# Performance work log

Measured on AMD Instinct MI355X. Metric: run time of the kernel, lower is better.

## Reference

```python
import jax, jax.numpy as jnp
import numpy as np
from jax import lax

EPS = 1e-5
NUM_HEADS = 8


def _safe_norm(x):
    # sqrt(max(sum x^2, EPS^2)) == max(||x||, EPS); grad-safe at 0
    return jnp.sqrt(jnp.maximum(jnp.sum(x * x, axis=-1, keepdims=True), EPS * EPS))


def _project(x):
    norm = _safe_norm(x)
    max_norm = 1.0 - EPS
    scale = jnp.where(norm >= max_norm, max_norm / (norm + EPS), jnp.ones_like(norm))
    return x * scale


def _logmap0(y):
    # logarithmic_map(0, y): lambda_0 = 2/(1+EPS)
    y = _project(y)
    n = _safe_norm(y)  # clamp(min=EPS) is built in
    lam = 2.0 / (1.0 + EPS)
    return (2.0 / lam) * jnp.arctanh(n) * (y / n)


def _expmap0(v):
    # exponential_map(0, v): lambda_0 = 2/(1+EPS)
    n = _safe_norm(v)
    lam = 2.0 / (1.0 + EPS)
    return _project(jnp.tanh(lam * n / 2.0) * (v / n))


def _mobius_add(x, y):
    x = _project(x)
    y = _project(y)
    xy = jnp.sum(x * y, axis=-1, keepdims=True)
    xn = jnp.sum(x * x, axis=-1, keepdims=True)
    yn = jnp.sum(y * y, axis=-1, keepdims=True)
    num = (1.0 + 2.0 * xy + yn) * x + (1.0 - xn) * y
    den = 1.0 + 2.0 * xy + xn * yn + EPS
    return _project(num / den)


def _hyp_linear(x, W, b):
    # HyperbolicLinear.forward: project -> logmap0 -> linear -> expmap0 -> mobius-add bias
    x = _project(x)
    xt = _logmap0(x)
    t = xt @ W.T
    r = _expmap0(t)
    r = _mobius_add(r, jnp.broadcast_to(b, r.shape))
    return r


def setup_inputs() -> dict:
    key = jax.random.key(0)
    ks = jax.random.split(key, 11)
    B, S, E = 4, 512, 512

    def xavier(k, shape):
        bound = np.sqrt(6.0 / (shape[0] + shape[1]))
        return jax.random.uniform(k, shape, jnp.float32, -bound, bound)

    return {
        "query": jax.random.normal(ks[0], (B, S, E), jnp.float32),
        "key": jax.random.normal(ks[1], (B, S, E), jnp.float32),
        "value": jax.random.normal(ks[2], (B, S, E), jnp.float32),
        "Wq": xavier(ks[3], (E, E)), "bq": 0.01 * jax.random.normal(ks[4], (E,), jnp.float32),
        "Wk": xavier(ks[5], (E, E)), "bk": 0.01 * jax.random.normal(ks[6], (E,), jnp.float32),
        "Wv": xavier(ks[7], (E, E)), "bv": 0.01 * jax.random.normal(ks[8], (E,), jnp.float32),
        "Wo": xavier(ks[9], (E, E)), "bo": 0.01 * jax.random.normal(ks[10], (E,), jnp.float32),
    }


def reference(query, key, value, Wq, bq, Wk, bk, Wv, bv, Wo, bo):
    B, S, E = query.shape
    H = NUM_HEADS
    D = E // H

    Q = _hyp_linear(query, Wq, bq).reshape(B, S, H, D).transpose(0, 2, 1, 3)  # [B,H,S,D]
    K = _hyp_linear(key, Wk, bk).reshape(B, S, H, D).transpose(0, 2, 1, 3)
    V = _hyp_linear(value, Wv, bv).reshape(B, S, H, D).transpose(0, 2, 1, 3)

    # Pairwise Poincare distance: d(q,k) = acosh(1 + 2||q-k||^2/((1-|q|^2)(1-|k|^2)) + EPS)
    q = _project(Q)
    k = _project(K)
    qn = jnp.sum(q * q, axis=-1)  # [B,H,S]
    kn = jnp.sum(k * k, axis=-1)  # [B,H,S]
    qk = jnp.einsum('bhqd,bhkd->bhqk', q, k)
    num = jnp.maximum(qn[..., :, None] + kn[..., None, :] - 2.0 * qk, 0.0)
    den = jnp.maximum((1.0 - qn)[..., :, None] * (1.0 - kn)[..., None, :], EPS)
    dist = jnp.arccosh(1.0 + 2.0 * num / den + EPS)  # [B,H,Sq,Sk]
    attn = jax.nn.softmax(-dist, axis=-1)

    # Sequential Mobius-add accumulation over key/value positions
    wt = jnp.moveaxis(attn, 3, 0)  # [Sk,B,H,Sq]
    vt = jnp.moveaxis(V, 2, 0)     # [Sk,B,H,D]

    @jax.checkpoint
    def step(ws, wv):
        wj, vj = wv  # wj: [B,H,Sq], vj: [B,H,D]
        return _mobius_add(ws, wj[..., None] * vj[:, :, None, :]), None

    ws0 = jnp.zeros((B, H, S, D), query.dtype)
    attended, _ = lax.scan(step, ws0, (wt, vt))  # [B,H,Sq,D]

    attended = attended.transpose(0, 2, 1, 3).reshape(B, S, E)
    return _hyp_linear(attended, Wo, bo)
```

## Files before the change

kernel.cpp:

```cpp
#include <hip/hip_runtime.h>
#include <math.h>

#define EPS  1e-5f
#define EPS2 1e-10f
#define MAXN (1.0f - EPS)

using short8  = __attribute__((ext_vector_type(8))) short;
using floatx4 = __attribute__((ext_vector_type(4))) float;
using float2v = __attribute__((ext_vector_type(2))) float;

template <int CTRL>
static __device__ __forceinline__ float qperm(float x) {
  return __int_as_float(__builtin_amdgcn_update_dpp(
      __float_as_int(x), __float_as_int(x), CTRL, 0xF, 0xF, false));
}
#define QP_XOR1    0xB1
#define QP_XOR2    0x4E
#define QP_HALFMIR 0x141

#if __has_builtin(__builtin_elementwise_fma)
static __device__ __forceinline__ float2v fma2(float2v a, float2v b, float2v c) {
  return __builtin_elementwise_fma(a, b, c);
}
#else
static __device__ __forceinline__ float2v fma2(float2v a, float2v b, float2v c) {
  float2v r; r.x = fmaf(a.x, b.x, c.x); r.y = fmaf(a.y, b.y, c.y); return r;
}
#endif

static __device__ __forceinline__ int pack_hi2(float a, float b) {
  return (int)((__float_as_uint(a) >> 16) | (__float_as_uint(b) & 0xFFFF0000u));
}
static __device__ __forceinline__ float hi_of(float a) {
  return __uint_as_float(__float_as_uint(a) & 0xFFFF0000u);
}

static __device__ __forceinline__ float logmap_f(float ss) {
  const float r = sqrtf(fmaxf(ss, EPS2));
  float at;
  if (r >= MAXN) {
    at = 0.5f * logf((r * (2.0f - EPS) + EPS) / (EPS * (1.0f + r)));
  } else {
    at = 0.5f * logf((1.0f + r) / (1.0f - r));
  }
  return (1.0f + EPS) * at / r;
}

__global__ __launch_bounds__(256) void k_gemm_mfma(
    const float* __restrict__ A0, const float* __restrict__ A1, const float* __restrict__ A2,
    const float* __restrict__ W0, const float* __restrict__ W1, const float* __restrict__ W2,
    float* __restrict__ Cbase) {
  const int z = blockIdx.z;
  const float* A = (z == 0) ? A0 : ((z == 1) ? A1 : A2);
  const float* W = (z == 0) ? W0 : ((z == 1) ? W1 : W2);
  float* C = Cbase + (size_t)z * (2048 * 512);
  __shared__ int Ahi[64][36], Alo[64][36], Whi[64][36], Wlo[64][36];
  __shared__ float f_lds[64];
  const int t = threadIdx.x;
  const int n0 = blockIdx.x * 64;
  const int m0 = blockIdx.y * 64;
  const int row = t >> 2, c0 = (t & 3) * 16, ci = (t & 3) * 8;
  const int w = t >> 6, lane = t & 63;
  const int quad = lane >> 4, l16 = lane & 15;
  const int mw = (w & 1) * 32, nw = (w >> 1) * 32;
  floatx4 acc[2][2];
#pragma unroll
  for (int i = 0; i < 2; ++i)
#pragma unroll
    for (int j = 0; j < 2; ++j) acc[i][j] = (floatx4){0.f, 0.f, 0.f, 0.f};
  float ssq = 0.0f;

  for (int k0 = 0; k0 < 512; k0 += 64) {
    float4 av[4], wv[4];
#pragma unroll
    for (int i = 0; i < 4; ++i) {
      av[i] = *(const float4*)&A[(size_t)(n0 + row) * 512 + k0 + c0 + 4 * i];
      wv[i] = *(const float4*)&W[(size_t)(m0 + row) * 512 + k0 + c0 + 4 * i];
    }
    int pAh[8], pAl[8], pWh[8], pWl[8];
#pragma unroll
    for (int i = 0; i < 4; ++i) {
      ssq = fmaf(av[i].x, av[i].x, ssq); ssq = fmaf(av[i].y, av[i].y, ssq);
      ssq = fmaf(av[i].z, av[i].z, ssq); ssq = fmaf(av[i].w, av[i].w, ssq);
      pAh[2 * i]     = pack_hi2(av[i].x, av[i].y);
      pAh[2 * i + 1] = pack_hi2(av[i].z, av[i].w);
      pAl[2 * i]     = pack_hi2(av[i].x - hi_of(av[i].x), av[i].y - hi_of(av[i].y));
      pAl[2 * i + 1] = pack_hi2(av[i].z - hi_of(av[i].z), av[i].w - hi_of(av[i].w));
      pWh[2 * i]     = pack_hi2(wv[i].x, wv[i].y);
      pWh[2 * i + 1] = pack_hi2(wv[i].z, wv[i].w);
      pWl[2 * i]     = pack_hi2(wv[i].x - hi_of(wv[i].x), wv[i].y - hi_of(wv[i].y));
      pWl[2 * i + 1] = pack_hi2(wv[i].z - hi_of(wv[i].z), wv[i].w - hi_of(wv[i].w));
    }
    __syncthreads();
    *(int4*)&Ahi[row][ci]     = *(int4*)&pAh[0];
    *(int4*)&Ahi[row][ci + 4] = *(int4*)&pAh[4];
    *(int4*)&Alo[row][ci]     = *(int4*)&pAl[0];
    *(int4*)&Alo[row][ci + 4] = *(int4*)&pAl[4];
    *(int4*)&Whi[row][ci]     = *(int4*)&pWh[0];
    *(int4*)&Whi[row][ci + 4] = *(int4*)&pWh[4];
    *(int4*)&Wlo[row][ci]     = *(int4*)&pWl[0];
    *(int4*)&Wlo[row][ci + 4] = *(int4*)&pWl[4];
    __syncthreads();
#pragma unroll
    for (int kk = 0; kk < 64; kk += 32) {
      short8 ah[2], al[2], bh[2], bl[2];
#pragma unroll
      for (int i = 0; i < 2; ++i) {
        ah[i] = *(const short8*)&((const short*)Ahi[mw + i * 16 + l16])[kk + quad * 8];
        al[i] = *(const short8*)&((const short*)Alo[mw + i * 16 + l16])[kk + quad * 8];
        bh[i] = *(const short8*)&((const short*)Whi[nw + i * 16 + l16])[kk + quad * 8];
        bl[i] = *(const short8*)&((const short*)Wlo[nw + i * 16 + l16])[kk + quad * 8];
      }
#pragma unroll
      for (int i = 0; i < 2; ++i)
#pragma unroll
        for (int j = 0; j < 2; ++j) {
          acc[i][j] = __builtin_amdgcn_mfma_f32_16x16x32_bf16(ah[i], bh[j], acc[i][j], 0, 0, 0);
          acc[i][j] = __builtin_amdgcn_mfma_f32_16x16x32_bf16(ah[i], bl[j], acc[i][j], 0, 0, 0);
          acc[i][j] = __builtin_amdgcn_mfma_f32_16x16x32_bf16(al[i], bh[j], acc[i][j], 0, 0, 0);
        }
    }
  }
  ssq += qperm<QP_XOR1>(ssq);
  ssq += qperm<QP_XOR2>(ssq);
  if ((t & 3) == 0) f_lds[row] = logmap_f(ssq);
  __syncthreads();
#pragma unroll
  for (int i = 0; i < 2; ++i) {
    const int lrow_base = mw + i * 16 + quad * 4;
#pragma unroll
    for (int r = 0; r < 4; ++r) {
      const float fv = f_lds[lrow_base + r];
#pragma unroll
      for (int j = 0; j < 2; ++j)
        C[(size_t)(n0 + lrow_base + r) * 512 + m0 + nw + j * 16 + l16] = fv * acc[i][j][r];
    }
  }
}

__global__ __launch_bounds__(256) void k_post(const float* __restrict__ tin,
                                              const float* __restrict__ b0,
                                              const float* __restrict__ b1,
                                              const float* __restrict__ b2,
                                              float* __restrict__ o0, float* __restrict__ o1,
                                              float* __restrict__ o2,
                                              float* __restrict__ nrm0, float* __restrict__ nrm1,
                                              float* __restrict__ nrm2,
                                              float* __restrict__ rowsum_init, int final_mode) {
  const int t = threadIdx.x;
  const int wv = t >> 6, lane = t & 63;
  const int nrow = blockIdx.x * 4 + wv;
  const int z = blockIdx.y;
  const float* tv = tin + ((size_t)z * 2048 + nrow) * 512;
  const float* bias = (z == 0) ? b0 : ((z == 1) ? b1 : b2);
  const int e0 = lane * 8;
  const float4 tp0 = *(const float4*)&tv[e0];
  const float4 tp1 = *(const float4*)&tv[e0 + 4];
  const float4 bp0 = *(const float4*)&bias[e0];
  const float4 bp1 = *(const float4*)&bias[e0 + 4];
  const float tpv[8] = {tp0.x, tp0.y, tp0.z, tp0.w, tp1.x, tp1.y, tp1.z, tp1.w};
  const float bpv[8] = {bp0.x, bp0.y, bp0.z, bp0.w, bp1.x, bp1.y, bp1.z, bp1.w};
  float p_tt = 0.f, p_tb = 0.f, p_bb = 0.f;
#pragma unroll
  for (int e = 0; e < 8; ++e) {
    p_tt = fmaf(tpv[e], tpv[e], p_tt);
    p_tb = fmaf(tpv[e], bpv[e], p_tb);
    p_bb = fmaf(bpv[e], bpv[e], p_bb);
  }
#pragma unroll
  for (int m = 32; m; m >>= 1) {
    p_tt += __shfl_xor(p_tt, m, 64);
    p_tb += __shfl_xor(p_tb, m, 64);
    p_bb += __shfl_xor(p_bb, m, 64);
  }
  const float s_tt = p_tt, s_tb = p_tb, s_bb = p_bb;
  const float tn = sqrtf(fmaxf(s_tt, EPS2));
  const float th = tanhf(tn / (1.0f + EPS));
  const float g = th / tn;
  const float rnorm = th * (sqrtf(s_tt) / tn);
  const float sr = (rnorm >= MAXN) ? (MAXN / (rnorm + EPS)) : 1.0f;
  const float gr = g * sr;
  const float rn = (rnorm * sr) * (rnorm * sr);
  const float bnorm = sqrtf(fmaxf(s_bb, EPS2));
  const float sb = (bnorm >= MAXN) ? (MAXN / (bnorm + EPS)) : 1.0f;
  const float xy = gr * sb * s_tb;
  const float yn = (sb * sb) * s_bb;
  const float Af = 1.0f + 2.0f * xy + yn;
  const float Cf = 1.0f - rn;
  const float den = 1.0f + 2.0f * xy + rn * yn + EPS;
  const float id = 1.0f / den;
  const float on_raw = (Af * Af * rn + 2.0f * Af * Cf * xy + Cf * Cf * yn) * (id * id);
  const float no = sqrtf(fmaxf(on_raw, EPS2));
  const float so = (no >= MAXN) ? (MAXN / (no + EPS)) : 1.0f;
  const float ms = id * so;
  const float ca = gr * Af * ms;
  const float cb = sb * Cf * ms;
  float v[8];
#pragma unroll
  for (int e = 0; e < 8; ++e) v[e] = ca * tpv[e] + cb * bpv[e];
  if (final_mode) {
    float4 oa; oa.x = v[0]; oa.y = v[1]; oa.z = v[2]; oa.w = v[3];
    float4 ob; ob.x = v[4]; ob.y = v[5]; ob.z = v[6]; ob.w = v[7];
    *(float4*)&o0[(size_t)nrow * 512 + e0] = oa;
    *(float4*)&o0[(size_t)nrow * 512 + e0 + 4] = ob;
    return;
  }
  float hp = 0.f;
#pragma unroll
  for (int e = 0; e < 8; ++e) hp = fmaf(v[e], v[e], hp);
  hp += __shfl_xor(hp, 1, 64);
  hp += __shfl_xor(hp, 2, 64);
  hp += __shfl_xor(hp, 4, 64);
  const float hnr = sqrtf(fmaxf(hp, EPS2));
  float sh = 1.0f;
  if (z != 2) sh = (hnr >= MAXN) ? (MAXN / (hnr + EPS)) : 1.0f;
  float* outz = (z == 0) ? o0 : ((z == 1) ? o1 : o2);
  float* nz = (z == 0) ? nrm0 : ((z == 1) ? nrm1 : nrm2);
  const int b = nrow >> 9, s = nrow & 511, h = lane >> 3, d = (lane & 7) * 8;
  float4 oa; oa.x = v[0] * sh; oa.y = v[1] * sh; oa.z = v[2] * sh; oa.w = v[3] * sh;
  float4 ob; ob.x = v[4] * sh; ob.y = v[5] * sh; ob.z = v[6] * sh; ob.w = v[7] * sh;
  float* op = &outz[(((size_t)(b * 8 + h) * 512 + s) * 64 + d)];
  *(float4*)&op[0] = oa;
  *(float4*)&op[4] = ob;
  if ((lane & 7) == 0) nz[(size_t)(b * 8 + h) * 512 + s] = hp * sh * sh;
  if (z == 0 && lane < 8) rowsum_init[((size_t)b * 8 + lane) * 512 + s] = 0.0f;
}

__global__ __launch_bounds__(256) void k_logits(const float* __restrict__ Q,
                                                const float* __restrict__ K,
                                                const float* __restrict__ qn,
                                                const float* __restrict__ kn,
                                                float* __restrict__ attn,
                                                float* __restrict__ rowsum) {
  const int bh = blockIdx.z;
  const int i0 = blockIdx.x * 64;
  const int j0 = blockIdx.y * 64;
  const float* Qb = Q + (size_t)bh * 512 * 64;
  const float* Kb = K + (size_t)bh * 512 * 64;
  __shared__ int Qhi[64][36], Qlo[64][36], Khi[64][36], Klo[64][36];
  const int t = threadIdx.x;
  const int row = t >> 2, c0 = (t & 3) * 16, ci = (t & 3) * 8;
  const int w = t >> 6, lane = t & 63;
  const int quad = lane >> 4, l16 = lane & 15;
  const int mw = (w & 1) * 32, nw = (w >> 1) * 32;
  float4 qv4[4], kv4[4];
#pragma unroll
  for (int i = 0; i < 4; ++i) {
    qv4[i] = *(const float4*)&Qb[(size_t)(i0 + row) * 64 + c0 + 4 * i];
    kv4[i] = *(const float4*)&Kb[(size_t)(j0 + row) * 64 + c0 + 4 * i];
  }
  int pQh[8], pQl[8], pKh[8], pKl[8];
#pragma unroll
  for (int i = 0; i < 4; ++i) {
    pQh[2 * i]     = pack_hi2(qv4[i].x, qv4[i].y);
    pQh[2 * i + 1] = pack_hi2(qv4[i].z, qv4[i].w);
    pQl[2 * i]     = pack_hi2(qv4[i].x - hi_of(qv4[i].x), qv4[i].y - hi_of(qv4[i].y));
    pQl[2 * i + 1] = pack_hi2(qv4[i].z - hi_of(qv4[i].z), qv4[i].w - hi_of(qv4[i].w));
    pKh[2 * i]     = pack_hi2(kv4[i].x, kv4[i].y);
    pKh[2 * i + 1] = pack_hi2(kv4[i].z, kv4[i].w);
    pKl[2 * i]     = pack_hi2(kv4[i].x - hi_of(kv4[i].x), kv4[i].y - hi_of(kv4[i].y));
    pKl[2 * i + 1] = pack_hi2(kv4[i].z - hi_of(kv4[i].z), kv4[i].w - hi_of(kv4[i].w));
  }
  *(int4*)&Qhi[row][ci]     = *(int4*)&pQh[0];
  *(int4*)&Qhi[row][ci + 4] = *(int4*)&pQh[4];
  *(int4*)&Qlo[row][ci]     = *(int4*)&pQl[0];
  *(int4*)&Qlo[row][ci + 4] = *(int4*)&pQl[4];
  *(int4*)&Khi[row][ci]     = *(int4*)&pKh[0];
  *(int4*)&Khi[row][ci + 4] = *(int4*)&pKh[4];
  *(int4*)&Klo[row][ci]     = *(int4*)&pKl[0];
  *(int4*)&Klo[row][ci + 4] = *(int4*)&pKl[4];
  __syncthreads();
  floatx4 acc[2][2];
#pragma unroll
  for (int i = 0; i < 2; ++i)
#pragma unroll
    for (int j = 0; j < 2; ++j) acc[i][j] = (floatx4){0.f, 0.f, 0.f, 0.f};
#pragma unroll
  for (int kk = 0; kk < 64; kk += 32) {
    short8 ah[2], al[2], bhv[2], blv[2];
#pragma unroll
    for (int i = 0; i < 2; ++i) {
      ah[i]  = *(const short8*)&((const short*)Qhi[mw + i * 16 + l16])[kk + quad * 8];
      al[i]  = *(const short8*)&((const short*)Qlo[mw + i * 16 + l16])[kk + quad * 8];
      bhv[i] = *(const short8*)&((const short*)Khi[nw + i * 16 + l16])[kk + quad * 8];
      blv[i] = *(const short8*)&((const short*)Klo[nw + i * 16 + l16])[kk + quad * 8];
    }
#pragma unroll
    for (int i = 0; i < 2; ++i)
#pragma unroll
      for (int j = 0; j < 2; ++j) {
        acc[i][j] = __builtin_amdgcn_mfma_f32_16x16x32_bf16(ah[i], bhv[j], acc[i][j], 0, 0, 0);
        acc[i][j] = __builtin_amdgcn_mfma_f32_16x16x32_bf16(ah[i], blv[j], acc[i][j], 0, 0, 0);
        acc[i][j] = __builtin_amdgcn_mfma_f32_16x16x32_bf16(al[i], bhv[j], acc[i][j], 0, 0, 0);
      }
  }
#pragma unroll
  for (int i = 0; i < 2; ++i) {
    float rs_acc[4] = {0.f, 0.f, 0.f, 0.f};
#pragma unroll
    for (int r = 0; r < 4; ++r) {
      const int grow = i0 + mw + i * 16 + quad * 4 + r;
      const float qni = qn[(size_t)bh * 512 + grow];
      const float rq = 1.0f - qni;
#pragma unroll
      for (int j = 0; j < 2; ++j) {
        const int gcol = j0 + nw + j * 16 + l16;
        const float knj = kn[(size_t)bh * 512 + gcol];
        const float num = fmaxf(qni + knj - 2.0f * acc[i][j][r], 0.0f);
        const float den = fmaxf(rq * (1.0f - knj), EPS);
        const float wv = fmaf(2.0f * num, __builtin_amdgcn_rcpf(den), EPS);
        const float s_ = 1.0f + wv + sqrtf(wv * (wv + 2.0f));
        const float rr = __builtin_amdgcn_rcpf(s_);
        rs_acc[r] += rr;
        attn[((size_t)bh * 512 + grow) * 512 + gcol] = rr;
      }
    }
#pragma unroll
    for (int r = 0; r < 4; ++r) {
      float v = rs_acc[r];
      v += __shfl_xor(v, 1, 64); v += __shfl_xor(v, 2, 64);
      v += __shfl_xor(v, 4, 64); v += __shfl_xor(v, 8, 64);
      if (l16 == 0)
        atomicAdd(&rowsum[(size_t)bh * 512 + i0 + mw + i * 16 + quad * 4 + r], v);
    }
  }
}

__global__ __launch_bounds__(256) void k_scan(const float* __restrict__ V,
                                              const float* __restrict__ vn,
                                              const float* __restrict__ rw,
                                              const float* __restrict__ rowsum,
                                              float* __restrict__ att) {
  __shared__ __align__(16) float v_lds[64 * 64];
  __shared__ __align__(16) float swyn_lds[64 * 66];
  __shared__ float g_lds[64];
  const int blk = blockIdx.x;
  const int bh = blk >> 4;
  const int i0 = (blk & 15) * 32;
  const int t = threadIdx.x;
  const int lane = t & 63, w = t >> 6;
  const int row_blk = w * 8 + (lane >> 3);
  const int sub = lane & 7;
  const int d0 = sub * 8;
  const float* Vb = V + (size_t)bh * 512 * 64;
  const float* vnb = vn + (size_t)bh * 512;
  const float* arow = rw + ((size_t)bh * 512 + i0 + row_blk) * 512;
  const float inv_s = __builtin_amdgcn_rcpf(rowsum[(size_t)bh * 512 + i0 + row_blk]);

  float2v wsv[4];
#pragma unroll
  for (int k = 0; k < 4; ++k) wsv[k] = (float2v){0.f, 0.f};
  float xn = 0.0f;

  for (int jc = 0; jc < 512; jc += 64) {
#pragma unroll
    for (int it = 0; it < 4; ++it) {
      const int idx4 = it * 256 + t;
      *(float4*)&v_lds[idx4 * 4] = *(const float4*)&Vb[(size_t)jc * 64 + idx4 * 4];
    }
    const float4 a0 = *(const float4*)&arow[jc + sub * 8];
    const float4 a1 = *(const float4*)&arow[jc + sub * 8 + 4];
    const float4 n0 = *(const float4*)&vnb[jc + sub * 8];
    const float4 n1 = *(const float4*)&vnb[jc + sub * 8 + 4];
    const float wq[8] = {a0.x, a0.y, a0.z, a0.w, a1.x, a1.y, a1.z, a1.w};
    const float nq[8] = {n0.x, n0.y, n0.z, n0.w, n1.x, n1.y, n1.z, n1.w};
#pragma unroll
    for (int e = 0; e < 8; ++e) {
      const float wgt = wq[e] * inv_s;
      float2 p; p.x = wgt; p.y = (wgt * wgt) * nq[e];
      *(float2*)&swyn_lds[(sub * 8 + e) * 66 + row_blk * 2] = p;
    }
    __syncthreads();

    {
      const int jg = row_blk * 2;
      const float4 va0 = *(const float4*)&v_lds[jg * 64 + d0];
      const float4 va1 = *(const float4*)&v_lds[jg * 64 + d0 + 4];
      const float4 vb0 = *(const float4*)&v_lds[(jg + 1) * 64 + d0];
      const float4 vb1 = *(const float4*)&v_lds[(jg + 1) * 64 + d0 + 4];
      const float4 vc0 = *(const float4*)&v_lds[((jg + 2) & 63) * 64 + d0];
      const float4 vc1 = *(const float4*)&v_lds[((jg + 2) & 63) * 64 + d0 + 4];
      float p0 = va0.x * vb0.x + va0.y * vb0.y + va0.z * vb0.z + va0.w * vb0.w +
                 va1.x * vb1.x + va1.y * vb1.y + va1.z * vb1.z + va1.w * vb1.w;
      float p1 = vb0.x * vc0.x + vb0.y * vc0.y + vb0.z * vc0.z + vb0.w * vc0.w +
                 vb1.x * vc1.x + vb1.y * vc1.y + vb1.z * vc1.z + vb1.w * vc1.w;
      p0 += qperm<QP_XOR1>(p0); p0 += qperm<QP_XOR2>(p0); p0 += qperm<QP_HALFMIR>(p0);
      p1 += qperm<QP_XOR1>(p1); p1 += qperm<QP_XOR2>(p1); p1 += qperm<QP_HALFMIR>(p1);
      if (sub == 0) { g_lds[jg] = p0; g_lds[jg + 1] = p1; }
    }
    float2v vcur[4];
    {
      const float4 c0v = *(const float4*)&v_lds[d0];
      const float4 c1v = *(const float4*)&v_lds[d0 + 4];
      vcur[0] = (float2v){c0v.x, c0v.y}; vcur[1] = (float2v){c0v.z, c0v.w};
      vcur[2] = (float2v){c1v.x, c1v.y}; vcur[3] = (float2v){c1v.z, c1v.w};
    }
    float2v dd = wsv[0] * vcur[0];
    dd = fma2(wsv[1], vcur[1], dd);
    dd = fma2(wsv[2], vcur[2], dd);
    dd = fma2(wsv[3], vcur[3], dd);
    float D = dd.x + dd.y;
    D += qperm<QP_XOR1>(D); D += qperm<QP_XOR2>(D); D += qperm<QP_HALFMIR>(D);
    __syncthreads();

#pragma unroll
    for (int j = 0; j < 64; ++j) {
      const float2 sy2 = *(const float2*)&swyn_lds[j * 66 + row_blk * 2];
      const float sw = sy2.x, yn = sy2.y;
      const float xnyn1 = fmaf(xn, yn, 1.0f + EPS);
      const float sxy   = xn + yn;
      const float ynp1  = 1.0f + yn;
      const float Cfsw  = (1.0f - xn) * sw;
      float2v vnx[4];
      float E = 0.0f;
      if (j < 63) {
        const float4 nx0 = *(const float4*)&v_lds[(j + 1) * 64 + d0];
        const float4 nx1 = *(const float4*)&v_lds[(j + 1) * 64 + d0 + 4];
        vnx[0] = (float2v){nx0.x, nx0.y}; vnx[1] = (float2v){nx0.z, nx0.w};
        vnx[2] = (float2v){nx1.x, nx1.y}; vnx[3] = (float2v){nx1.z, nx1.w};
        float2v ee = wsv[0] * vnx[0];
        ee = fma2(wsv[1], vnx[1], ee);
        ee = fma2(wsv[2], vnx[2], ee);
        ee = fma2(wsv[3], vnx[3], ee);
        E = ee.x + ee.y;
        E += qperm<QP_XOR1>(E); E += qperm<QP_XOR2>(E); E += qperm<QP_HALFMIR>(E);
      }
      const float xy  = sw * D;
      const float den = fmaf(2.0f, xy, xnyn1);
      const float s2  = fmaf(2.0f, xy, sxy);
      const float Af  = fmaf(2.0f, xy, ynp1);
      const float id  = __builtin_amdgcn_rcpf(den);
      const float dn  = den - EPS;
      const float am  = Af * id;
      const float cm  = Cfsw * id;
      xn = (s2 * id) * (dn * id);
      const float2v amv = {am, am};
      const float2v cmv = {cm, cm};
      wsv[0] = fma2(amv, wsv[0], cmv * vcur[0]);
      wsv[1] = fma2(amv, wsv[1], cmv * vcur[1]);
      wsv[2] = fma2(amv, wsv[2], cmv * vcur[2]);
      wsv[3] = fma2(amv, wsv[3], cmv * vcur[3]);
      if (j < 63) {
        D = fmaf(am, E, cm * g_lds[j]);
        vcur[0] = vnx[0]; vcur[1] = vnx[1]; vcur[2] = vnx[2]; vcur[3] = vnx[3];
      }
    }
    __syncthreads();
  }
  const int b = bh >> 3, h = bh & 7;
  float* o = att + (((size_t)b * 512 + i0 + row_blk) * 512 + h * 64 + d0);
  float4 s0; s0.x = wsv[0].x; s0.y = wsv[0].y; s0.z = wsv[1].x; s0.w = wsv[1].y;
  float4 s1; s1.x = wsv[2].x; s1.y = wsv[2].y; s1.z = wsv[3].x; s1.w = wsv[3].y;
  *(float4*)&o[0] = s0;
  *(float4*)&o[4] = s1;
}

extern "C" void kernel_launch(void* const* d_in, const int* in_sizes, int n_in,
                              void* d_out, int out_size, void* d_ws, size_t ws_size,
                              hipStream_t stream) {
  const float* query = (const float*)d_in[0];
  const float* key_  = (const float*)d_in[1];
  const float* value = (const float*)d_in[2];
  const float* Wq = (const float*)d_in[3];
  const float* bq = (const float*)d_in[4];
  const float* Wk = (const float*)d_in[5];
  const float* bk = (const float*)d_in[6];
  const float* Wv = (const float*)d_in[7];
  const float* bv = (const float*)d_in[8];
  const float* Wo = (const float*)d_in[9];
  const float* bo = (const float*)d_in[10];
  float* ws = (float*)d_ws;
  const size_t M = 1u << 20;
  float* Qb     = ws;
  float* Kb     = ws + 1 * M;
  float* Vb     = ws + 2 * M;
  float* qn     = ws + 3 * M;
  float* kn     = qn + 16384;
  float* vn     = kn + 16384;
  float* rowsum = vn + 16384;
  float* rw     = ws + 4 * M;
  float* t3     = ws + 12 * M;
  float* att    = ws + 15 * M;
  float* to_    = ws + 16 * M;

  k_gemm_mfma<<<dim3(32, 8, 3), 256, 0, stream>>>(query, key_, value, Wq, Wk, Wv, t3);
  k_post<<<dim3(512, 3), 256, 0, stream>>>(t3, bq, bk, bv, Qb, Kb, Vb, qn, kn, vn,
                                           rowsum, 0);
  k_logits<<<dim3(8, 8, 32), 256, 0, stream>>>(Qb, Kb, qn, kn, rw, rowsum);
  k_scan<<<512, 256, 0, stream>>>(Vb, vn, rw, rowsum, att);
  k_gemm_mfma<<<dim3(32, 8, 1), 256, 0, stream>>>(att, att, att, Wo, Wo, Wo, to_);
  k_post<<<dim3(512, 1), 256, 0, stream>>>(to_, bo, bo, bo, (float*)d_out,
                                           nullptr, nullptr, nullptr, nullptr, nullptr,
                                           nullptr, 1);
}
```

Baseline: 232.9 us.

## Pre-split inputs and weights into bf16 hi/lo planes in separate kernels

Adds a k_split kernel that converts activations and weights into packed bf16 hi/lo arrays once, and computes the logmap row scale factors there. The GEMM and logits kernels now load the pre-split shorts directly into LDS instead of splitting fp32 tiles on every block. k_post also emits Q/K as hi/lo bf16. This removes redundant per-tile conversion and the weight re-splitting repeated across row blocks, at the cost of extra kernel launches and an extra global round trip for the split data.

```diff
diff --git a/kernel.cpp b/kernel.cpp
--- a/kernel.cpp
+++ b/kernel.cpp
@@ -46,20 +46,56 @@
   return (1.0f + EPS) * at / r;
 }
 
-__global__ __launch_bounds__(256) void k_gemm_mfma(
-    const float* __restrict__ A0, const float* __restrict__ A1, const float* __restrict__ A2,
-    const float* __restrict__ W0, const float* __restrict__ W1, const float* __restrict__ W2,
-    float* __restrict__ Cbase) {
+__global__ __launch_bounds__(256) void k_split(const float* __restrict__ s0,
+                                               const float* __restrict__ s1,
+                                               const float* __restrict__ s2,
+                                               const float* __restrict__ s3,
+                                               short* __restrict__ hi,
+                                               short* __restrict__ lo,
+                                               float* __restrict__ f, int rows_per) {
+  const int z = blockIdx.y, t = threadIdx.x;
+  const int wv = t >> 6, lane = t & 63;
+  const int row = blockIdx.x * 4 + wv;
+  const float* src = (z == 0) ? s0 : ((z == 1) ? s1 : ((z == 2) ? s2 : s3));
+  const float* rp = src + (size_t)row * 512 + lane * 8;
+  const float4 a = *(const float4*)&rp[0];
+  const float4 b = *(const float4*)&rp[4];
+  const float v[8] = {a.x, a.y, a.z, a.w, b.x, b.y, b.z, b.w};
+  int h4[4], l4[4];
+#pragma unroll
+  for (int i = 0; i < 4; ++i) {
+    h4[i] = pack_hi2(v[2 * i], v[2 * i + 1]);
+    l4[i] = pack_hi2(v[2 * i] - hi_of(v[2 * i]), v[2 * i + 1] - hi_of(v[2 * i + 1]));
+  }
+  const size_t off = ((size_t)z * rows_per + row) * 512 + lane * 8;
+  *(int4*)&hi[off] = *(int4*)h4;
+  *(int4*)&lo[off] = *(int4*)l4;
+  if (f) {
+    float ssq = 0.f;
+#pragma unroll
+    for (int e = 0; e < 8; ++e) ssq = fmaf(v[e], v[e], ssq);
+#pragma unroll
+    for (int m = 32; m; m >>= 1) ssq += __shfl_xor(ssq, m, 64);
+    if (lane == 0) f[z * rows_per + row] = logmap_f(ssq);
+  }
+}
+
+__global__ __launch_bounds__(256) void k_gemm_pre(
+    const short* __restrict__ Ahi, const short* __restrict__ Alo,
+    const short* __restrict__ Whi, const short* __restrict__ Wlo,
+    const float* __restrict__ f, float* __restrict__ Cbase) {
   const int z = blockIdx.z;
-  const float* A = (z == 0) ? A0 : ((z == 1) ? A1 : A2);
-  const float* W = (z == 0) ? W0 : ((z == 1) ? W1 : W2);
+  const short* Ah_ = Ahi + (size_t)z * (2048 * 512);
+  const short* Al_ = Alo + (size_t)z * (2048 * 512);
+  const short* Wh_ = Whi + (size_t)z * (512 * 512);
+  const short* Wl_ = Wlo + (size_t)z * (512 * 512);
+  const float* fz = f + z * 2048;
   float* C = Cbase + (size_t)z * (2048 * 512);
-  __shared__ int Ahi[64][36], Alo[64][36], Whi[64][36], Wlo[64][36];
-  __shared__ float f_lds[64];
+  __shared__ short Ah[64][72], Al[64][72], Wh[64][72], Wl[64][72];
   const int t = threadIdx.x;
   const int n0 = blockIdx.x * 64;
   const int m0 = blockIdx.y * 64;
-  const int row = t >> 2, c0 = (t & 3) * 16, ci = (t & 3) * 8;
+  const int row = t >> 2, c0 = (t & 3) * 16;
   const int w = t >> 6, lane = t & 63;
   const int quad = lane >> 4, l16 = lane & 15;
   const int mw = (w & 1) * 32, nw = (w >> 1) * 32;
@@ -68,48 +104,31 @@
   for (int i = 0; i < 2; ++i)
 #pragma unroll
     for (int j = 0; j < 2; ++j) acc[i][j] = (floatx4){0.f, 0.f, 0.f, 0.f};
-  float ssq = 0.0f;
 
   for (int k0 = 0; k0 < 512; k0 += 64) {
-    float4 av[4], wv[4];
-#pragma unroll
-    for (int i = 0; i < 4; ++i) {
-      av[i] = *(const float4*)&A[(size_t)(n0 + row) * 512 + k0 + c0 + 4 * i];
-      wv[i] = *(const float4*)&W[(size_t)(m0 + row) * 512 + k0 + c0 + 4 * i];
-    }
-    int pAh[8], pAl[8], pWh[8], pWl[8];
-#pragma unroll
-    for (int i = 0; i < 4; ++i) {
-      ssq = fmaf(av[i].x, av[i].x, ssq); ssq = fmaf(av[i].y, av[i].y, ssq);
-      ssq = fmaf(av[i].z, av[i].z, ssq); ssq = fmaf(av[i].w, av[i].w, ssq);
-      pAh[2 * i]     = pack_hi2(av[i].x, av[i].y);
-      pAh[2 * i + 1] = pack_hi2(av[i].z, av[i].w);
-      pAl[2 * i]     = pack_hi2(av[i].x - hi_of(av[i].x), av[i].y - hi_of(av[i].y));
-      pAl[2 * i + 1] = pack_hi2(av[i].z - hi_of(av[i].z), av[i].w - hi_of(av[i].w));
-      pWh[2 * i]     = pack_hi2(wv[i].x, wv[i].y);
-      pWh[2 * i + 1] = pack_hi2(wv[i].z, wv[i].w);
-      pWl[2 * i]     = pack_hi2(wv[i].x - hi_of(wv[i].x), wv[i].y - hi_of(wv[i].y));
-      pWl[2 * i + 1] = pack_hi2(wv[i].z - hi_of(wv[i].z), wv[i].w - hi_of(wv[i].w));
-    }
+    const short8 a0 = *(const short8*)&Ah_[(size_t)(n0 + row) * 512 + k0 + c0];
+    const short8 a1 = *(const short8*)&Ah_[(size_t)(n0 + row) * 512 + k0 + c0 + 8];
+    const short8 b0 = *(const short8*)&Al_[(size_t)(n0 + row) * 512 + k0 + c0];
+    const short8 b1 = *(const short8*)&Al_[(size_t)(n0 + row) * 512 + k0 + c0 + 8];
+    const short8 c0v = *(const short8*)&Wh_[(size_t)(m0 + row) * 512 + k0 + c0];
+    const short8 c1v = *(const short8*)&Wh_[(size_t)(m0 + row) * 512 + k0 + c0 + 8];
+    const short8 d0v = *(const short8*)&Wl_[(size_t)(m0 + row) * 512 + k0 + c0];
+    const short8 d1v = *(const short8*)&Wl_[(size_t)(m0 + row) * 512 + k0 + c0 + 8];
     __syncthreads();
-    *(int4*)&Ahi[row][ci]     = *(int4*)&pAh[0];
-    *(int4*)&Ahi[row][ci + 4] = *(int4*)&pAh[4];
-    *(int4*)&Alo[row][ci]     = *(int4*)&pAl[0];
-    *(int4*)&Alo[row][ci + 4] = *(int4*)&pAl[4];
-    *(int4*)&Whi[row][ci]     = *(int4*)&pWh[0];
-    *(int4*)&Whi[row][ci + 4] = *(int4*)&pWh[4];
-    *(int4*)&Wlo[row][ci]     = *(int4*)&pWl[0];
-    *(int4*)&Wlo[row][ci + 4] = *(int4*)&pWl[4];
+    *(short8*)&Ah[row][c0] = a0; *(short8*)&Ah[row][c0 + 8] = a1;
+    *(short8*)&Al[row][c0] = b0; *(short8*)&Al[row][c0 + 8] = b1;
+    *(short8*)&Wh[row][c0] = c0v; *(short8*)&Wh[row][c0 + 8] = c1v;
+    *(short8*)&Wl[row][c0] = d0v; *(short8*)&Wl[row][c0 + 8] = d1v;
     __syncthreads();
 #pragma unroll
     for (int kk = 0; kk < 64; kk += 32) {
       short8 ah[2], al[2], bh[2], bl[2];
 #pragma unroll
       for (int i = 0; i < 2; ++i) {
-        ah[i] = *(const short8*)&((const short*)Ahi[mw + i * 16 + l16])[kk + quad * 8];
-        al[i] = *(const short8*)&((const short*)Alo[mw + i * 16 + l16])[kk + quad * 8];
-        bh[i] = *(const short8*)&((const short*)Whi[nw + i * 16 + l16])[kk + quad * 8];
-        bl[i] = *(const short8*)&((const short*)Wlo[nw + i * 16 + l16])[kk + quad * 8];
+        ah[i] = *(const short8*)&Ah[mw + i * 16 + l16][kk + quad * 8];
+        al[i] = *(const short8*)&Al[mw + i * 16 + l16][kk + quad * 8];
+        bh[i] = *(const short8*)&Wh[nw + i * 16 + l16][kk + quad * 8];
+        bl[i] = *(const short8*)&Wl[nw + i * 16 + l16][kk + quad * 8];
       }
 #pragma unroll
       for (int i = 0; i < 2; ++i)
@@ -121,16 +140,12 @@
         }
     }
   }
-  ssq += qperm<QP_XOR1>(ssq);
-  ssq += qperm<QP_XOR2>(ssq);
-  if ((t & 3) == 0) f_lds[row] = logmap_f(ssq);
-  __syncthreads();
 #pragma unroll
   for (int i = 0; i < 2; ++i) {
     const int lrow_base = mw + i * 16 + quad * 4;
 #pragma unroll
     for (int r = 0; r < 4; ++r) {
-      const float fv = f_lds[lrow_base + r];
+      const float fv = fz[n0 + lrow_base + r];
 #pragma unroll
       for (int j = 0; j < 2; ++j)
         C[(size_t)(n0 + lrow_base + r) * 512 + m0 + nw + j * 16 + l16] = fv * acc[i][j][r];
@@ -142,10 +157,11 @@
                                               const float* __restrict__ b0,
                                               const float* __restrict__ b1,
                                               const float* __restrict__ b2,
-                                              float* __restrict__ o0, float* __restrict__ o1,
-                                              float* __restrict__ o2,
-                                              float* __restrict__ nrm0, float* __restrict__ nrm1,
-                                              float* __restrict__ nrm2,
+                                              short* __restrict__ Qhi, short* __restrict__ Qlo,
+                                              short* __restrict__ Khi, short* __restrict__ Klo,
+                                              float* __restrict__ Vb, float* __restrict__ ofin,
+                                              float* __restrict__ qn, float* __restrict__ kn,
+                                              float* __restrict__ vn,
                                               float* __restrict__ rowsum_init, int final_mode) {
   const int t = threadIdx.x;
   const int wv = t >> 6, lane = t & 63;
@@ -201,8 +217,8 @@
   if (final_mode) {
     float4 oa; oa.x = v[0]; oa.y = v[1]; oa.z = v[2]; oa.w = v[3];
     float4 ob; ob.x = v[4]; ob.y = v[5]; ob.z = v[6]; ob.w = v[7];
-    *(float4*)&o0[(size_t)nrow * 512 + e0] = oa;
-    *(float4*)&o0[(size_t)nrow * 512 + e0 + 4] = ob;
+    *(float4*)&ofin[(size_t)nrow * 512 + e0] = oa;
+    *(float4*)&ofin[(size_t)nrow * 512 + e0 + 4] = ob;
     return;
   }
   float hp = 0.f;
@@ -214,20 +230,38 @@
   const float hnr = sqrtf(fmaxf(hp, EPS2));
   float sh = 1.0f;
   if (z != 2) sh = (hnr >= MAXN) ? (MAXN / (hnr + EPS)) : 1.0f;
-  float* outz = (z == 0) ? o0 : ((z == 1) ? o1 : o2);
-  float* nz = (z == 0) ? nrm0 : ((z == 1) ? nrm1 : nrm2);
   const int b = nrow >> 9, s = nrow & 511, h = lane >> 3, d = (lane & 7) * 8;
-  float4 oa; oa.x = v[0] * sh; oa.y = v[1] * sh; oa.z = v[2] * sh; oa.w = v[3] * sh;
-  float4 ob; ob.x = v[4] * sh; ob.y = v[5] * sh; ob.z = v[6] * sh; ob.w = v[7] * sh;
-  float* op = &outz[(((size_t)(b * 8 + h) * 512 + s) * 64 + d)];
-  *(float4*)&op[0] = oa;
-  *(float4*)&op[4] = ob;
-  if ((lane & 7) == 0) nz[(size_t)(b * 8 + h) * 512 + s] = hp * sh * sh;
+  const size_t off = (((size_t)(b * 8 + h) * 512 + s) * 64 + d);
+  float vv[8];
+#pragma unroll
+  for (int e = 0; e < 8; ++e) vv[e] = v[e] * sh;
+  if (z == 2) {
+    float4 oa; oa.x = vv[0]; oa.y = vv[1]; oa.z = vv[2]; oa.w = vv[3];
+    float4 ob; ob.x = vv[4]; ob.y = vv[5]; ob.z = vv[6]; ob.w = vv[7];
+    *(float4*)&Vb[off] = oa;
+    *(float4*)&Vb[off + 4] = ob;
+    if ((lane & 7) == 0) vn[(size_t)(b * 8 + h) * 512 + s] = hp;
+  } else {
+    short* hz = (z == 0) ? Qhi : Khi;
+    short* lz = (z == 0) ? Qlo : Klo;
+    int h4[4], l4[4];
+#pragma unroll
+    for (int i = 0; i < 4; ++i) {
+      h4[i] = pack_hi2(vv[2 * i], vv[2 * i + 1]);
+      l4[i] = pack_hi2(vv[2 * i] - hi_of(vv[2 * i]), vv[2 * i + 1] - hi_of(vv[2 * i + 1]));
+    }
+    *(int4*)&hz[off] = *(int4*)h4;
+    *(int4*)&lz[off] = *(int4*)l4;
+    float* nz = (z == 0) ? qn : kn;
+    if ((lane & 7) == 0) nz[(size_t)(b * 8 + h) * 512 + s] = hp * sh * sh;
+  }
   if (z == 0 && lane < 8) rowsum_init[((size_t)b * 8 + lane) * 512 + s] = 0.0f;
 }
 
-__global__ __launch_bounds__(256) void k_logits(const float* __restrict__ Q,
-                                                const float* __restrict__ K,
+__global__ __launch_bounds__(256) void k_logits(const short* __restrict__ Qhi,
+                                                const short* __restrict__ Qlo,
+                                                const short* __restrict__ Khi,
+                                                const short* __restrict__ Klo,
                                                 const float* __restrict__ qn,
                                                 const float* __restrict__ kn,
                                                 float* __restrict__ attn,
@@ -235,40 +269,28 @@
   const int bh = blockIdx.z;
   const int i0 = blockIdx.x * 64;
   const int j0 = blockIdx.y * 64;
-  const float* Qb = Q + (size_t)bh * 512 * 64;
-  const float* Kb = K + (size_t)bh * 512 * 64;
-  __shared__ int Qhi[64][36], Qlo[64][36], Khi[64][36], Klo[64][36];
+  const short* Qh_ = Qhi + (size_t)bh * 512 * 64;
+  const short* Ql_ = Qlo + (size_t)bh * 512 * 64;
+  const short* Kh_ = Khi + (size_t)bh * 512 * 64;
+  const short* Kl_ = Klo + (size_t)bh * 512 * 64;
+  __shared__ short Qh[64][72], Ql[64][72], Kh[64][72], Kl[64][72];
   const int t = threadIdx.x;
-  const int row = t >> 2, c0 = (t & 3) * 16, ci = (t & 3) * 8;
+  const int row = t >> 2, c0 = (t & 3) * 16;
   const int w = t >> 6, lane = t & 63;
   const int quad = lane >> 4, l16 = lane & 15;
   const int mw = (w & 1) * 32, nw = (w >> 1) * 32;
-  float4 qv4[4], kv4[4];
-#pragma unroll
-  for (int i = 0; i < 4; ++i) {
-    qv4[i] = *(const float4*)&Qb[(size_t)(i0 + row) * 64 + c0 + 4 * i];
-    kv4[i] = *(const float4*)&Kb[(size_t)(j0 + row) * 64 + c0 + 4 * i];
-  }
-  int pQh[8], pQl[8], pKh[8], pKl[8];
-#pragma unroll
-  for (int i = 0; i < 4; ++i) {
-    pQh[2 * i]     = pack_hi2(qv4[i].x, qv4[i].y);
-    pQh[2 * i + 1] = pack_hi2(qv4[i].z, qv4[i].w);
-    pQl[2 * i]     = pack_hi2(qv4[i].x - hi_of(qv4[i].x), qv4[i].y - hi_of(qv4[i].y));
-    pQl[2 * i + 1] = pack_hi2(qv4[i].z - hi_of(qv4[i].z), qv4[i].w - hi_of(qv4[i].w));
-    pKh[2 * i]     = pack_hi2(kv4[i].x, kv4[i].y);
-    pKh[2 * i + 1] = pack_hi2(kv4[i].z, kv4[i].w);
-    pKl[2 * i]     = pack_hi2(kv4[i].x - hi_of(kv4[i].x), kv4[i].y - hi_of(kv4[i].y));
-    pKl[2 * i + 1] = pack_hi2(kv4[i].z - hi_of(kv4[i].z), kv4[i].w - hi_of(kv4[i].w));
-  }
-  *(int4*)&Qhi[row][ci]     = *(int4*)&pQh[0];
-  *(int4*)&Qhi[row][ci + 4] = *(int4*)&pQh[4];
-  *(int4*)&Qlo[row][ci]     = *(int4*)&pQl[0];
-  *(int4*)&Qlo[row][ci + 4] = *(int4*)&pQl[4];
-  *(int4*)&Khi[row][ci]     = *(int4*)&pKh[0];
-  *(int4*)&Khi[row][ci + 4] = *(int4*)&pKh[4];
-  *(int4*)&Klo[row][ci]     = *(int4*)&pKl[0];
-  *(int4*)&Klo[row][ci + 4] = *(int4*)&pKl[4];
+  const short8 q0 = *(const short8*)&Qh_[(size_t)(i0 + row) * 64 + c0];
+  const short8 q1 = *(const short8*)&Qh_[(size_t)(i0 + row) * 64 + c0 + 8];
+  const short8 q2 = *(const short8*)&Ql_[(size_t)(i0 + row) * 64 + c0];
+  const short8 q3 = *(const short8*)&Ql_[(size_t)(i0 + row) * 64 + c0 + 8];
+  const short8 k0v = *(const short8*)&Kh_[(size_t)(j0 + row) * 64 + c0];
+  const short8 k1v = *(const short8*)&Kh_[(size_t)(j0 + row) * 64 + c0 + 8];
+  const short8 k2v = *(const short8*)&Kl_[(size_t)(j0 + row) * 64 + c0];
+  const short8 k3v = *(const short8*)&Kl_[(size_t)(j0 + row) * 64 + c0 + 8];
+  *(short8*)&Qh[row][c0] = q0; *(short8*)&Qh[row][c0 + 8] = q1;
+  *(short8*)&Ql[row][c0] = q2; *(short8*)&Ql[row][c0 + 8] = q3;
+  *(short8*)&Kh[row][c0] = k0v; *(short8*)&Kh[row][c0 + 8] = k1v;
+  *(short8*)&Kl[row][c0] = k2v; *(short8*)&Kl[row][c0 + 8] = k3v;
   __syncthreads();
   floatx4 acc[2][2];
 #pragma unroll
@@ -280,10 +302,10 @@
     short8 ah[2], al[2], bhv[2], blv[2];
 #pragma unroll
     for (int i = 0; i < 2; ++i) {
-      ah[i]  = *(const short8*)&((const short*)Qhi[mw + i * 16 + l16])[kk + quad * 8];
-      al[i]  = *(const short8*)&((const short*)Qlo[mw + i * 16 + l16])[kk + quad * 8];
-      bhv[i] = *(const short8*)&((const short*)Khi[nw + i * 16 + l16])[kk + quad * 8];
-      blv[i] = *(const short8*)&((const short*)Klo[nw + i * 16 + l16])[kk + quad * 8];
+      ah[i]  = *(const short8*)&Qh[mw + i * 16 + l16][kk + quad * 8];
+      al[i]  = *(const short8*)&Ql[mw + i * 16 + l16][kk + quad * 8];
+      bhv[i] = *(const short8*)&Kh[nw + i * 16 + l16][kk + quad * 8];
+      blv[i] = *(const short8*)&Kl[nw + i * 16 + l16][kk + quad * 8];
     }
 #pragma unroll
     for (int i = 0; i < 2; ++i)
@@ -471,25 +493,39 @@
   const float* bo = (const float*)d_in[10];
   float* ws = (float*)d_ws;
   const size_t M = 1u << 20;
-  float* Qb     = ws;
-  float* Kb     = ws + 1 * M;
-  float* Vb     = ws + 2 * M;
-  float* qn     = ws + 3 * M;
-  float* kn     = qn + 16384;
-  float* vn     = kn + 16384;
+  short* Qhi = (short*)(ws);
+  short* Qlo = (short*)(ws + (M >> 1));
+  short* Khi = (short*)(ws + M);
+  short* Klo = (short*)(ws + M + (M >> 1));
+  float* Vb  = ws + 2 * M;
+  float* qn  = ws + 3 * M;
+  float* kn  = qn + 16384;
+  float* vn  = kn + 16384;
   float* rowsum = vn + 16384;
-  float* rw     = ws + 4 * M;
-  float* t3     = ws + 12 * M;
-  float* att    = ws + 15 * M;
-  float* to_    = ws + 16 * M;
-
-  k_gemm_mfma<<<dim3(32, 8, 3), 256, 0, stream>>>(query, key_, value, Wq, Wk, Wv, t3);
-  k_post<<<dim3(512, 3), 256, 0, stream>>>(t3, bq, bk, bv, Qb, Kb, Vb, qn, kn, vn,
-                                           rowsum, 0);
-  k_logits<<<dim3(8, 8, 32), 256, 0, stream>>>(Qb, Kb, qn, kn, rw, rowsum);
+  float* f3  = rowsum + 16384;
+  float* fo  = f3 + 3 * 2048;
+  float* rw  = ws + 4 * M;
+  short* Ahi3 = (short*)(ws + 4 * M);
+  short* Alo3 = (short*)(ws + 4 * M + M + (M >> 1));
+  short* atthi = (short*)(ws + 4 * M);
+  short* attlo = (short*)(ws + 4 * M + (M >> 1));
+  float* t3  = ws + 12 * M;
+  float* att = ws + 15 * M;
+  float* to_ = ws + 16 * M;
+  short* Whi4 = (short*)(ws + 17 * M);
+  short* Wlo4 = (short*)(ws + 17 * M + (M >> 1));
+
+  k_split<<<dim3(512, 3), 256, 0, stream>>>(query, key_, value, nullptr, Ahi3, Alo3, f3, 2048);
+  k_split<<<dim3(128, 4), 256, 0, stream>>>(Wq, Wk, Wv, Wo, Whi4, Wlo4, nullptr, 512);
+  k_gemm_pre<<<dim3(32, 8, 3), 256, 0, stream>>>(Ahi3, Alo3, Whi4, Wlo4, f3, t3);
+  k_post<<<dim3(512, 3), 256, 0, stream>>>(t3, bq, bk, bv, Qhi, Qlo, Khi, Klo, Vb,
+                                           nullptr, qn, kn, vn, rowsum, 0);
+  k_logits<<<dim3(8, 8, 32), 256, 0, stream>>>(Qhi, Qlo, Khi, Klo, qn, kn, rw, rowsum);
   k_scan<<<512, 256, 0, stream>>>(Vb, vn, rw, rowsum, att);
-  k_gemm_mfma<<<dim3(32, 8, 1), 256, 0, stream>>>(att, att, att, Wo, Wo, Wo, to_);
-  k_post<<<dim3(512, 1), 256, 0, stream>>>(to_, bo, bo, bo, (float*)d_out,
-                                           nullptr, nullptr, nullptr, nullptr, nullptr,
-                                           nullptr, 1);
-}
+  k_split<<<dim3(512, 1), 256, 0, stream>>>(att, att, att, att, atthi, attlo, fo, 2048);
+  k_gemm_pre<<<dim3(32, 8, 1), 256, 0, stream>>>(atthi, attlo, Whi4 + 3 * 512 * 512,
+                                                 Wlo4 + 3 * 512 * 512, fo, to_);
+  k_post<<<dim3(512, 1), 256, 0, stream>>>(to_, bo, bo, bo, nullptr, nullptr, nullptr,
+                                           nullptr, nullptr, (float*)d_out,
+                                           nullptr, nullptr, nullptr, nullptr, 1);
+}
```

Result: no change. 236.6 us (+1.6%).
